# Kernel optimization log

Measured on AMD Instinct MI355X. Metric: run time of the kernel, lower is better.

## Reference

```python
import jax, jax.numpy as jnp
import numpy as np

N_NODES = 40000
N_EDGES = 640000
D_IN = 128
D_OUT = 128


def setup_inputs() -> dict:
    key = jax.random.key(0)
    k1, k2, k3 = jax.random.split(key, 3)
    x = jax.random.normal(k1, (N_NODES, D_IN), dtype=jnp.float32)
    W = jax.random.normal(k2, (D_IN, D_OUT), dtype=jnp.float32) / np.sqrt(D_IN)
    b = jnp.zeros((D_OUT,), dtype=jnp.float32)
    edge_index = jax.random.randint(k3, (2, N_EDGES), 0, N_NODES, dtype=jnp.int64)
    return {"x": x, "W": W, "b": b, "edge_index": edge_index}


def reference(x, W, b, edge_index):
    src, dst = edge_index[0], edge_index[1]
    n = x.shape[0]
    # asymmetric normalization: 1 / out-degree(src), inf -> 0
    deg = jax.ops.segment_sum(jnp.ones_like(src, dtype=x.dtype), src, num_segments=n)
    deg_inv = jnp.where(deg > 0, 1.0 / deg, 0.0)
    # GCNConv (add_self_loops=False, normalize=False): h = x @ W; msg_e = w_e * h[src_e]
    h = x @ W  # [N, D_OUT]
    msg = h[src] * deg_inv[src][:, None]  # [E, D_OUT] gather-weighted messages
    out = jax.ops.segment_sum(msg, dst, num_segments=n) + b  # scatter-add to dst
    return out
```

## Files before the change

kernel.cpp:

```cpp
#include <hip/hip_runtime.h>

#define N_NODES 40000
#define D 128
#define N_EDGES 640000
#define GRP 128
#define NKEY 313
#define P1TILE 2048
#define P1BLKS 313
#define NSLICE 32
#define SLICE_E 20000
#define SLICE_E4 5000
#define HALF_BINS 20000
#define HALF_W 10000
#define WROW 20000
#define SRCH_BLKS 64
#define GEMM_BLKS 625
#define XPAD 132

typedef __attribute__((ext_vector_type(8))) short short8_t;
typedef __attribute__((ext_vector_type(4))) float float4_t;

static __device__ __forceinline__ unsigned short f2bf(float f) {
  unsigned u = __float_as_uint(f);
  return (unsigned short)((u + 0x7fffu + ((u >> 16) & 1u)) >> 16);
}
static __device__ __forceinline__ float bf2f(unsigned short h) {
  return __uint_as_float(((unsigned)h) << 16);
}

static __device__ __forceinline__ void scan512(unsigned* s, int tid) {
  const int t2 = tid + 256;
#pragma unroll
  for (int off = 1; off < 512; off <<= 1) {
    unsigned a = (tid >= off) ? s[tid - off] : 0u;
    unsigned c = (t2 >= off) ? s[t2 - off] : 0u;
    __syncthreads();
    s[tid] += a;
    s[t2] += c;
    __syncthreads();
  }
}

__global__ __launch_bounds__(256) void k_prep(const float* __restrict__ W,
                                              unsigned short* __restrict__ Wb) {
  const int g = blockIdx.x * 256 + threadIdx.x;
  const int j = g & 7;
  const int lane = (g >> 3) & 63;
  const int q = (g >> 9) & 3;
  const int t = g >> 11;
  const int k = q * 32 + (lane >> 4) * 8 + j;
  const int d = t * 16 + (lane & 15);
  Wb[g] = f2bf(W[k * D + d]);
}

__global__ __launch_bounds__(256) void k1(
    const float* __restrict__ x, const unsigned short* __restrict__ Wb,
    const int* __restrict__ src, const int* __restrict__ dst,
    unsigned* __restrict__ slabS, unsigned* __restrict__ slabP,
    unsigned short* __restrict__ hb) {
  __shared__ unsigned smem[10240];
  const int bid = blockIdx.x;
  const int tid = threadIdx.x;

  if (bid < SRCH_BLKS) {
    const int b = bid >> 1;
    const int h = bid & 1;
    for (int i = tid; i < HALF_W; i += 256) smem[i] = 0;
    __syncthreads();
    const int4* p4 = (const int4*)(src + b * SLICE_E);
    const unsigned lo = (unsigned)(h * HALF_BINS);
    for (int it = tid; it < SLICE_E4; it += 256) {
      const int4 v = p4[it];
      unsigned u;
      u = (unsigned)v.x - lo; if (u < HALF_BINS) atomicAdd(&smem[u >> 1], 1u << ((u & 1) * 16));
      u = (unsigned)v.y - lo; if (u < HALF_BINS) atomicAdd(&smem[u >> 1], 1u << ((u & 1) * 16));
      u = (unsigned)v.z - lo; if (u < HALF_BINS) atomicAdd(&smem[u >> 1], 1u << ((u & 1) * 16));
      u = (unsigned)v.w - lo; if (u < HALF_BINS) atomicAdd(&smem[u >> 1], 1u << ((u & 1) * 16));
    }
    __syncthreads();
    unsigned* row = slabS + (size_t)b * WROW + h * HALF_W;
    for (int i = tid; i < HALF_W; i += 256) row[i] = smem[i];
    return;
  }

  const int t = bid - SRCH_BLKS;
  if (t % 3 == 2) {
    const int cid = t / 3;
    unsigned* cnt = smem;
    const int t2 = tid + 256;
    if (tid < NKEY) cnt[tid] = 0;
    if (t2 < NKEY) cnt[t2] = 0;
    __syncthreads();
    const int e0 = cid * P1TILE + tid * 8;
    if (e0 < N_EDGES) {
      const int4 da = *(const int4*)(dst + e0);
      const int4 db = *(const int4*)(dst + e0 + 4);
      atomicAdd(&cnt[da.x >> 7], 1u);
      atomicAdd(&cnt[da.y >> 7], 1u);
      atomicAdd(&cnt[da.z >> 7], 1u);
      atomicAdd(&cnt[da.w >> 7], 1u);
      atomicAdd(&cnt[db.x >> 7], 1u);
      atomicAdd(&cnt[db.y >> 7], 1u);
      atomicAdd(&cnt[db.z >> 7], 1u);
      atomicAdd(&cnt[db.w >> 7], 1u);
    }
    __syncthreads();
    if (tid < NKEY) slabP[(size_t)cid * NKEY + tid] = cnt[tid];
    if (t2 < NKEY) slabP[(size_t)cid * NKEY + t2] = cnt[t2];
    return;
  }

  const int gid = 2 * (t / 3) + (t % 3);
  if (gid >= GEMM_BLKS) return;
  const int n0 = gid * 64;
  const int w = tid >> 6;
  const int lane = tid & 63;

  float* xl = (float*)smem;
  {
    const float4* xg = (const float4*)(x + (size_t)n0 * D);
#pragma unroll
    for (int j = 0; j < 8; ++j) {
      const int idx = tid + j * 256;
      const int row = idx >> 5;
      const int c4 = idx & 31;
      ((float4*)(xl + row * XPAD))[c4] = xg[idx];
    }
  }
  __syncthreads();

  short8_t afrag[4];
  {
    const float* ap0 = xl + (w * 16 + (lane & 15)) * XPAD + (lane >> 4) * 8;
#pragma unroll
    for (int q = 0; q < 4; ++q) {
      const float* ap = ap0 + q * 32;
      const float4 v0 = *(const float4*)ap;
      const float4 v1 = *(const float4*)(ap + 4);
      short8_t a;
      a[0] = (short)f2bf(v0.x); a[1] = (short)f2bf(v0.y);
      a[2] = (short)f2bf(v0.z); a[3] = (short)f2bf(v0.w);
      a[4] = (short)f2bf(v1.x); a[5] = (short)f2bf(v1.y);
      a[6] = (short)f2bf(v1.z); a[7] = (short)f2bf(v1.w);
      afrag[q] = a;
    }
  }

  const int orow = n0 + w * 16 + (lane >> 4) * 4;
  const int ocolbase = lane & 15;
#pragma unroll
  for (int t8 = 0; t8 < 8; ++t8) {
    float4_t acc = {0.f, 0.f, 0.f, 0.f};
#pragma unroll
    for (int q = 0; q < 4; ++q) {
      const short8_t bfrag =
          *(const short8_t*)(Wb + ((size_t)(t8 * 4 + q) * 64 + lane) * 8);
      acc = __builtin_amdgcn_mfma_f32_16x16x32_bf16(afrag[q], bfrag, acc, 0, 0, 0);
    }
    const int col = t8 * 16 + ocolbase;
#pragma unroll
    for (int r = 0; r < 4; ++r)
      hb[(size_t)(orow + r) * D + col] = f2bf(acc[r]);
  }
}

__global__ __launch_bounds__(256) void k2(
    const unsigned* __restrict__ slabP, const unsigned* __restrict__ slabS,
    unsigned* __restrict__ rowbase, unsigned* __restrict__ keytotal,
    float* __restrict__ dinv) {
  const int bid = blockIdx.x;
  const int tid = threadIdx.x;
  if (bid < NKEY) {
    const int k = bid;
    __shared__ unsigned s[512];
    const int t2 = tid + 256;
    unsigned v0 = slabP[(size_t)tid * NKEY + k];
    unsigned v1 = (t2 < NKEY) ? slabP[(size_t)t2 * NKEY + k] : 0u;
    s[tid] = v0;
    s[t2] = v1;
    __syncthreads();
    scan512(s, tid);
    rowbase[(size_t)tid * NKEY + k] = s[tid] - v0;
    if (t2 < NKEY) rowbase[(size_t)t2 * NKEY + k] = s[t2] - v1;
    if (tid == 0) keytotal[k] = s[NKEY - 1];
    return;
  }
  const int w = (bid - NKEY) * 256 + tid;
  if (w >= WROW) return;
  unsigned run = 0;
#pragma unroll 8
  for (int b = 0; b < NSLICE; ++b) run += slabS[(size_t)b * WROW + w];
  const unsigned lo = run & 0xFFFFu;
  const unsigned hi = run >> 16;
  dinv[2 * w] = lo ? 1.0f / (float)lo : 0.0f;
  dinv[2 * w + 1] = hi ? 1.0f / (float)hi : 0.0f;
}

__global__ __launch_bounds__(256) void k3(
    const int* __restrict__ src, const int* __restrict__ dst,
    const unsigned* __restrict__ rowbase, const unsigned* __restrict__ keytotal,
    unsigned* __restrict__ epack) {
  __shared__ unsigned s[512];
  __shared__ unsigned ko[NKEY];
  __shared__ unsigned rb[NKEY];
  __shared__ unsigned cnt[NKEY];
  const int b = blockIdx.x;
  const int tid = threadIdx.x;
  const int t2 = tid + 256;

  unsigned kv0 = (tid < NKEY) ? keytotal[tid] : 0u;
  unsigned kv1 = (t2 < NKEY) ? keytotal[t2] : 0u;
  s[tid] = kv0;
  s[t2] = kv1;
  if (tid < NKEY) { rb[tid] = rowbase[(size_t)b * NKEY + tid]; cnt[tid] = 0; }
  if (t2 < NKEY) { rb[t2] = rowbase[(size_t)b * NKEY + t2]; cnt[t2] = 0; }
  __syncthreads();
  scan512(s, tid);
  if (tid < NKEY) ko[tid] = s[tid] - kv0;
  if (t2 < NKEY) ko[t2] = s[t2] - kv1;
  __syncthreads();

  const int e0 = b * P1TILE + tid * 8;
  if (e0 < N_EDGES) {
    const int4 sa = *(const int4*)(src + e0);
    const int4 sb = *(const int4*)(src + e0 + 4);
    const int4 da = *(const int4*)(dst + e0);
    const int4 db = *(const int4*)(dst + e0 + 4);
#define PLACE(DV, SV)                                                   \
  {                                                                     \
    const int d_ = (DV);                                                \
    const int k_ = d_ >> 7;                                             \
    const unsigned lr_ = atomicAdd(&cnt[k_], 1u);                       \
    epack[ko[k_] + rb[k_] + lr_] =                                      \
        ((unsigned)(d_ & 127) << 16) | (unsigned)(SV);                  \
  }
    PLACE(da.x, sa.x) PLACE(da.y, sa.y) PLACE(da.z, sa.z) PLACE(da.w, sa.w)
    PLACE(db.x, sb.x) PLACE(db.y, sb.y) PLACE(db.z, sb.z) PLACE(db.w, sb.w)
#undef PLACE
  }
}

__global__ __launch_bounds__(256) void k4a(
    const unsigned* __restrict__ keytotal, const unsigned* __restrict__ epack,
    int* __restrict__ offs, int* __restrict__ cnt_dst,
    unsigned short* __restrict__ esrc16) {
  __shared__ unsigned s[512];
  __shared__ unsigned cnt[GRP];
  __shared__ unsigned loc[GRP];
  __shared__ unsigned cur[GRP];
  __shared__ unsigned sstart, slen;
  const int k = blockIdx.x;
  const int tid = threadIdx.x;
  const int t2 = tid + 256;

  unsigned kv0 = (tid < NKEY) ? keytotal[tid] : 0u;
  unsigned kv1 = (t2 < NKEY) ? keytotal[t2] : 0u;
  s[tid] = kv0;
  s[t2] = kv1;
  if (tid < GRP) cnt[tid] = 0;
  __syncthreads();
  scan512(s, tid);
  if (tid == 0) {
    sstart = s[k] - keytotal[k];
    slen = keytotal[k];
  }
  __syncthreads();
  const unsigned start = sstart;
  const unsigned len = slen;

  for (unsigned i = tid; i < len; i += 256) {
    atomicAdd(&cnt[epack[start + i] >> 16], 1u);
  }
  __syncthreads();

  unsigned v = (tid < GRP) ? cnt[tid] : 0u;
  s[tid] = v;
  __syncthreads();
#pragma unroll
  for (int off = 1; off < 256; off <<= 1) {
    unsigned a = (tid >= off) ? s[tid - off] : 0u;
    __syncthreads();
    s[tid] += a;
    __syncthreads();
  }
  if (tid < GRP) {
    const unsigned ex = s[tid] - v;
    loc[tid] = ex;
    cur[tid] = ex;
    const int n = k * GRP + tid;
    if (n < N_NODES) {
      offs[n] = (int)(start + ex);
      cnt_dst[n] = (int)v;
    }
  }
  __syncthreads();

  for (unsigned i = tid; i < len; i += 256) {
    const unsigned p = epack[start + i];
    const unsigned dl = p >> 16;
    const unsigned r = atomicAdd(&cur[dl], 1u);
    esrc16[start + r] = (unsigned short)(p & 0xFFFFu);
  }
}

__global__ __launch_bounds__(256) void k4b(
    const int* __restrict__ offs, const int* __restrict__ cnt_dst,
    const float* __restrict__ dinv, const unsigned short* __restrict__ esrc16,
    const unsigned short* __restrict__ hb,
    const float* __restrict__ b, float* __restrict__ out) {
  const int tid = threadIdx.x;
  const int node = blockIdx.x * 8 + (tid >> 5);
  const int lane = tid & 31;

  const int start = offs[node];
  const int len = cnt_dst[node];
  const unsigned short* bk = esrc16 + start;

  float4 a0 = {0.f, 0.f, 0.f, 0.f};
  float4 a1 = {0.f, 0.f, 0.f, 0.f};
  float4 a2 = {0.f, 0.f, 0.f, 0.f};
  float4 a3 = {0.f, 0.f, 0.f, 0.f};

  int j = 0;
  for (; j + 3 < len; j += 4) {
    const int s0 = bk[j + 0];
    const int s1 = bk[j + 1];
    const int s2 = bk[j + 2];
    const int s3 = bk[j + 3];
    const float f0 = dinv[s0];
    const float f1 = dinv[s1];
    const float f2 = dinv[s2];
    const float f3 = dinv[s3];
    ushort4 u0 = ((const ushort4*)(hb + (size_t)s0 * D))[lane];
    ushort4 u1 = ((const ushort4*)(hb + (size_t)s1 * D))[lane];
    ushort4 u2 = ((const ushort4*)(hb + (size_t)s2 * D))[lane];
    ushort4 u3 = ((const ushort4*)(hb + (size_t)s3 * D))[lane];
    a0.x += f0 * bf2f(u0.x); a0.y += f0 * bf2f(u0.y); a0.z += f0 * bf2f(u0.z); a0.w += f0 * bf2f(u0.w);
    a1.x += f1 * bf2f(u1.x); a1.y += f1 * bf2f(u1.y); a1.z += f1 * bf2f(u1.z); a1.w += f1 * bf2f(u1.w);
    a2.x += f2 * bf2f(u2.x); a2.y += f2 * bf2f(u2.y); a2.z += f2 * bf2f(u2.z); a2.w += f2 * bf2f(u2.w);
    a3.x += f3 * bf2f(u3.x); a3.y += f3 * bf2f(u3.y); a3.z += f3 * bf2f(u3.z); a3.w += f3 * bf2f(u3.w);
  }
  for (; j < len; ++j) {
    const int s0 = bk[j];
    const float f0 = dinv[s0];
    ushort4 u0 = ((const ushort4*)(hb + (size_t)s0 * D))[lane];
    a0.x += f0 * bf2f(u0.x); a0.y += f0 * bf2f(u0.y); a0.z += f0 * bf2f(u0.z); a0.w += f0 * bf2f(u0.w);
  }

  const float4 bias = ((const float4*)b)[lane];
  float4 v;
  v.x = bias.x + (a0.x + a1.x) + (a2.x + a3.x);
  v.y = bias.y + (a0.y + a1.y) + (a2.y + a3.y);
  v.z = bias.z + (a0.z + a1.z) + (a2.z + a3.z);
  v.w = bias.w + (a0.w + a1.w) + (a2.w + a3.w);
  ((float4*)(out + (size_t)node * D))[lane] = v;
}

extern "C" void kernel_launch(void* const* d_in, const int* in_sizes, int n_in,
                              void* d_out, int out_size, void* d_ws, size_t ws_size,
                              hipStream_t stream) {
  const float* x = (const float*)d_in[0];
  const float* W = (const float*)d_in[1];
  const float* b = (const float*)d_in[2];
  const int* ei = (const int*)d_in[3];
  const int* src = ei;
  const int* dst = ei + N_EDGES;
  float* out = (float*)d_out;

  char* ws = (char*)d_ws;
  float* dinv = (float*)(ws + 0);
  unsigned* slabS = (unsigned*)(ws + 160000);
  unsigned short* Wb = (unsigned short*)(ws + 2720000);
  unsigned* slabP = (unsigned*)(ws + 2752768);
  unsigned* rowbase = (unsigned*)(ws + 3144960);
  unsigned* keytotal = (unsigned*)(ws + 3537152);
  unsigned* epack = (unsigned*)(ws + 3541248);
  int* offs = (int*)(ws + 6101248);
  int* cnt_dst = (int*)(ws + 6261248);
  unsigned short* esrc16 = (unsigned short*)(ws + 6421248);
  unsigned short* hb = (unsigned short*)(ws + 7701248);

  k_prep<<<64, 256, 0, stream>>>(W, Wb);
  k1<<<SRCH_BLKS + 939, 256, 0, stream>>>(x, Wb, src, dst, slabS, slabP, hb);
  k2<<<NKEY + 79, 256, 0, stream>>>(slabP, slabS, rowbase, keytotal, dinv);
  k3<<<P1BLKS, 256, 0, stream>>>(src, dst, rowbase, keytotal, epack);
  k4a<<<NKEY, 256, 0, stream>>>(keytotal, epack, offs, cnt_dst, esrc16);
  k4b<<<5000, 256, 0, stream>>>(offs, cnt_dst, dinv, esrc16, hb, b, out);
}
```

Measured before the change: 73.39 us.

## Fuse W bf16 packing into GEMM blocks and shuffle-broadcast edge indices in gather

Drops the separate k_prep launch. Each GEMM block of k1 now converts W to bf16 in the MFMA fragment layout in LDS, and x is stored as bf16 in LDS so the A fragments load directly. In the aggregation kernel, each lane loads one neighbor index and its dinv, and these are broadcast with __shfl for the first 32 edges, with 8 row gathers in flight at a time. This removes a launch and the redundant scalar index and dinv loads. In exchange every one of the 625 GEMM blocks re-reads and re-converts all of W, and LDS per block grows, which may reduce occupancy.

```diff
diff --git a/kernel.cpp b/kernel.cpp
--- a/kernel.cpp
+++ b/kernel.cpp
@@ -15,7 +15,7 @@
 #define WROW 20000
 #define SRCH_BLKS 64
 #define GEMM_BLKS 625
-#define XPAD 132
+#define XP 136
 
 typedef __attribute__((ext_vector_type(8))) short short8_t;
 typedef __attribute__((ext_vector_type(4))) float float4_t;
@@ -41,24 +41,12 @@
   }
 }
 
-__global__ __launch_bounds__(256) void k_prep(const float* __restrict__ W,
-                                              unsigned short* __restrict__ Wb) {
-  const int g = blockIdx.x * 256 + threadIdx.x;
-  const int j = g & 7;
-  const int lane = (g >> 3) & 63;
-  const int q = (g >> 9) & 3;
-  const int t = g >> 11;
-  const int k = q * 32 + (lane >> 4) * 8 + j;
-  const int d = t * 16 + (lane & 15);
-  Wb[g] = f2bf(W[k * D + d]);
-}
-
 __global__ __launch_bounds__(256) void k1(
-    const float* __restrict__ x, const unsigned short* __restrict__ Wb,
+    const float* __restrict__ x, const float* __restrict__ W,
     const int* __restrict__ src, const int* __restrict__ dst,
     unsigned* __restrict__ slabS, unsigned* __restrict__ slabP,
     unsigned short* __restrict__ hb) {
-  __shared__ unsigned smem[10240];
+  __shared__ unsigned smem[12544];
   const int bid = blockIdx.x;
   const int tid = threadIdx.x;
 
@@ -116,7 +104,24 @@
   const int w = tid >> 6;
   const int lane = tid & 63;
 
-  float* xl = (float*)smem;
+  unsigned short* wb = (unsigned short*)smem;
+  unsigned short* xb = wb + 16384;
+
+#pragma unroll 4
+  for (int i = 0; i < 16; ++i) {
+    const int g4 = i * 256 + tid;
+    const int k = g4 >> 5;
+    const int d0 = (g4 & 31) * 4;
+    const float4 v = ((const float4*)W)[g4];
+    const int q = k >> 5, r = k & 31;
+    const int base =
+        (((d0 >> 4) * 4 + q) * 64 + ((r >> 3) * 16 + (d0 & 15))) * 8 + (r & 7);
+    wb[base] = f2bf(v.x);
+    wb[base + 8] = f2bf(v.y);
+    wb[base + 16] = f2bf(v.z);
+    wb[base + 24] = f2bf(v.w);
+  }
+
   {
     const float4* xg = (const float4*)(x + (size_t)n0 * D);
 #pragma unroll
@@ -124,26 +129,19 @@
       const int idx = tid + j * 256;
       const int row = idx >> 5;
       const int c4 = idx & 31;
-      ((float4*)(xl + row * XPAD))[c4] = xg[idx];
+      const float4 v = xg[idx];
+      ushort4 o;
+      o.x = f2bf(v.x); o.y = f2bf(v.y); o.z = f2bf(v.z); o.w = f2bf(v.w);
+      *(ushort4*)(xb + row * XP + c4 * 4) = o;
     }
   }
   __syncthreads();
 
   short8_t afrag[4];
   {
-    const float* ap0 = xl + (w * 16 + (lane & 15)) * XPAD + (lane >> 4) * 8;
-#pragma unroll
-    for (int q = 0; q < 4; ++q) {
-      const float* ap = ap0 + q * 32;
-      const float4 v0 = *(const float4*)ap;
-      const float4 v1 = *(const float4*)(ap + 4);
-      short8_t a;
-      a[0] = (short)f2bf(v0.x); a[1] = (short)f2bf(v0.y);
-      a[2] = (short)f2bf(v0.z); a[3] = (short)f2bf(v0.w);
-      a[4] = (short)f2bf(v1.x); a[5] = (short)f2bf(v1.y);
-      a[6] = (short)f2bf(v1.z); a[7] = (short)f2bf(v1.w);
-      afrag[q] = a;
-    }
+    const unsigned short* ap0 = xb + (w * 16 + (lane & 15)) * XP + (lane >> 4) * 8;
+#pragma unroll
+    for (int q = 0; q < 4; ++q) afrag[q] = *(const short8_t*)(ap0 + q * 32);
   }
 
   const int orow = n0 + w * 16 + (lane >> 4) * 4;
@@ -153,8 +151,7 @@
     float4_t acc = {0.f, 0.f, 0.f, 0.f};
 #pragma unroll
     for (int q = 0; q < 4; ++q) {
-      const short8_t bfrag =
-          *(const short8_t*)(Wb + ((size_t)(t8 * 4 + q) * 64 + lane) * 8);
+      const short8_t bfrag = *(const short8_t*)(wb + ((t8 * 4 + q) * 64 + lane) * 8);
       acc = __builtin_amdgcn_mfma_f32_16x16x32_bf16(afrag[q], bfrag, acc, 0, 0, 0);
     }
     const int col = t8 * 16 + ocolbase;
@@ -246,7 +243,6 @@
     unsigned short* __restrict__ esrc16) {
   __shared__ unsigned s[512];
   __shared__ unsigned cnt[GRP];
-  __shared__ unsigned loc[GRP];
   __shared__ unsigned cur[GRP];
   __shared__ unsigned sstart, slen;
   const int k = blockIdx.x;
@@ -285,7 +281,6 @@
   }
   if (tid < GRP) {
     const unsigned ex = s[tid] - v;
-    loc[tid] = ex;
     cur[tid] = ex;
     const int n = k * GRP + tid;
     if (n < N_NODES) {
@@ -316,43 +311,54 @@
   const int len = cnt_dst[node];
   const unsigned short* bk = esrc16 + start;
 
-  float4 a0 = {0.f, 0.f, 0.f, 0.f};
-  float4 a1 = {0.f, 0.f, 0.f, 0.f};
-  float4 a2 = {0.f, 0.f, 0.f, 0.f};
-  float4 a3 = {0.f, 0.f, 0.f, 0.f};
-
-  int j = 0;
-  for (; j + 3 < len; j += 4) {
-    const int s0 = bk[j + 0];
-    const int s1 = bk[j + 1];
-    const int s2 = bk[j + 2];
-    const int s3 = bk[j + 3];
-    const float f0 = dinv[s0];
-    const float f1 = dinv[s1];
-    const float f2 = dinv[s2];
-    const float f3 = dinv[s3];
-    ushort4 u0 = ((const ushort4*)(hb + (size_t)s0 * D))[lane];
-    ushort4 u1 = ((const ushort4*)(hb + (size_t)s1 * D))[lane];
-    ushort4 u2 = ((const ushort4*)(hb + (size_t)s2 * D))[lane];
-    ushort4 u3 = ((const ushort4*)(hb + (size_t)s3 * D))[lane];
-    a0.x += f0 * bf2f(u0.x); a0.y += f0 * bf2f(u0.y); a0.z += f0 * bf2f(u0.z); a0.w += f0 * bf2f(u0.w);
-    a1.x += f1 * bf2f(u1.x); a1.y += f1 * bf2f(u1.y); a1.z += f1 * bf2f(u1.z); a1.w += f1 * bf2f(u1.w);
-    a2.x += f2 * bf2f(u2.x); a2.y += f2 * bf2f(u2.y); a2.z += f2 * bf2f(u2.z); a2.w += f2 * bf2f(u2.w);
-    a3.x += f3 * bf2f(u3.x); a3.y += f3 * bf2f(u3.y); a3.z += f3 * bf2f(u3.z); a3.w += f3 * bf2f(u3.w);
-  }
-  for (; j < len; ++j) {
-    const int s0 = bk[j];
-    const float f0 = dinv[s0];
-    ushort4 u0 = ((const ushort4*)(hb + (size_t)s0 * D))[lane];
-    a0.x += f0 * bf2f(u0.x); a0.y += f0 * bf2f(u0.y); a0.z += f0 * bf2f(u0.z); a0.w += f0 * bf2f(u0.w);
+  int sj = 0;
+  if (lane < len) sj = bk[lane];
+  const float fj = dinv[sj];
+
+  float4 aa[4];
+#pragma unroll
+  for (int q = 0; q < 4; ++q) aa[q] = make_float4(0.f, 0.f, 0.f, 0.f);
+
+  const int l32 = len < 32 ? len : 32;
+  for (int jj = 0; jj < l32; jj += 8) {
+    ushort4 u[8];
+    float fq[8];
+#pragma unroll
+    for (int q = 0; q < 8; ++q) {
+      const int j = jj + q;
+      const int s = __shfl(sj, j, 32);
+      const float f = __shfl(fj, j, 32);
+      const bool on = j < l32;
+      const int ss = on ? s : 0;
+      u[q] = ((const ushort4*)(hb + (size_t)ss * D))[lane];
+      fq[q] = on ? f : 0.0f;
+    }
+#pragma unroll
+    for (int q = 0; q < 8; ++q) {
+      const float f = fq[q];
+      float4& a = aa[q & 3];
+      a.x += f * bf2f(u[q].x);
+      a.y += f * bf2f(u[q].y);
+      a.z += f * bf2f(u[q].z);
+      a.w += f * bf2f(u[q].w);
+    }
+  }
+  for (int j = 32; j < len; ++j) {
+    const int s = bk[j];
+    const float f = dinv[s];
+    ushort4 u = ((const ushort4*)(hb + (size_t)s * D))[lane];
+    aa[0].x += f * bf2f(u.x);
+    aa[0].y += f * bf2f(u.y);
+    aa[0].z += f * bf2f(u.z);
+    aa[0].w += f * bf2f(u.w);
   }
 
   const float4 bias = ((const float4*)b)[lane];
   float4 v;
-  v.x = bias.x + (a0.x + a1.x) + (a2.x + a3.x);
-  v.y = bias.y + (a0.y + a1.y) + (a2.y + a3.y);
-  v.z = bias.z + (a0.z + a1.z) + (a2.z + a3.z);
-  v.w = bias.w + (a0.w + a1.w) + (a2.w + a3.w);
+  v.x = bias.x + (aa[0].x + aa[1].x) + (aa[2].x + aa[3].x);
+  v.y = bias.y + (aa[0].y + aa[1].y) + (aa[2].y + aa[3].y);
+  v.z = bias.z + (aa[0].z + aa[1].z) + (aa[2].z + aa[3].z);
+  v.w = bias.w + (aa[0].w + aa[1].w) + (aa[2].w + aa[3].w);
   ((float4*)(out + (size_t)node * D))[lane] = v;
 }
 
@@ -370,18 +376,16 @@
   char* ws = (char*)d_ws;
   float* dinv = (float*)(ws + 0);
   unsigned* slabS = (unsigned*)(ws + 160000);
-  unsigned short* Wb = (unsigned short*)(ws + 2720000);
-  unsigned* slabP = (unsigned*)(ws + 2752768);
-  unsigned* rowbase = (unsigned*)(ws + 3144960);
-  unsigned* keytotal = (unsigned*)(ws + 3537152);
-  unsigned* epack = (unsigned*)(ws + 3541248);
-  int* offs = (int*)(ws + 6101248);
-  int* cnt_dst = (int*)(ws + 6261248);
-  unsigned short* esrc16 = (unsigned short*)(ws + 6421248);
-  unsigned short* hb = (unsigned short*)(ws + 7701248);
-
-  k_prep<<<64, 256, 0, stream>>>(W, Wb);
-  k1<<<SRCH_BLKS + 939, 256, 0, stream>>>(x, Wb, src, dst, slabS, slabP, hb);
+  unsigned* slabP = (unsigned*)(ws + 2720000);
+  unsigned* rowbase = (unsigned*)(ws + 3112192);
+  unsigned* keytotal = (unsigned*)(ws + 3504384);
+  unsigned* epack = (unsigned*)(ws + 3508480);
+  int* offs = (int*)(ws + 6068480);
+  int* cnt_dst = (int*)(ws + 6228480);
+  unsigned short* esrc16 = (unsigned short*)(ws + 6388480);
+  unsigned short* hb = (unsigned short*)(ws + 7668480);
+
+  k1<<<SRCH_BLKS + 939, 256, 0, stream>>>(x, W, src, dst, slabS, slabP, hb);
   k2<<<NKEY + 79, 256, 0, stream>>>(slabP, slabS, rowbase, keytotal, dinv);
   k3<<<P1BLKS, 256, 0, stream>>>(src, dst, rowbase, keytotal, epack);
   k4a<<<NKEY, 256, 0, stream>>>(keytotal, epack, offs, cnt_dst, esrc16);
```

Measured after the change: 66.23 us. 9.8% less time.
